# Kernel tuning notes

Hardware: AMD Instinct MI355X
Metric: run time of the kernel (lower is better)

The kernel has to match this reference:

```python
import jax, jax.numpy as jnp
import numpy as np

D_MODEL = 1024
N_HEADS = 16
WINDOW = 128
B, N, M = 2, 2048, 2048


def _linear_params(key, d_in, d_out):
    kw, kb = jax.random.split(key)
    lim = 1.0 / np.sqrt(d_in)
    w = jax.random.uniform(kw, (d_out, d_in), jnp.float32, -lim, lim)
    b = jax.random.uniform(kb, (d_out,), jnp.float32, -lim, lim)
    return w, b


def setup_inputs() -> dict:
    key = jax.random.key(0)
    ks = jax.random.split(key, 7)
    queries = jax.random.normal(ks[0], (B, N, D_MODEL), jnp.float32)
    keys = jax.random.normal(ks[1], (B, M, D_MODEL), jnp.float32)
    values = jax.random.normal(ks[2], (B, M, D_MODEL), jnp.float32)
    wq, bq = _linear_params(ks[3], D_MODEL, D_MODEL)
    wk, bk = _linear_params(ks[4], D_MODEL, D_MODEL)
    wv, bv = _linear_params(ks[5], D_MODEL, D_MODEL)
    wo, bo = _linear_params(ks[6], D_MODEL, D_MODEL)
    return {"queries": queries, "keys": keys, "values": values,
            "wq": wq, "bq": bq, "wk": wk, "bk": bk,
            "wv": wv, "bv": bv, "wo": wo, "bo": bo}


def reference(queries, keys, values, wq, bq, wk, bk, wv, bv, wo, bo):
    b, n, d = queries.shape
    m = keys.shape[1]
    h = N_HEADS
    hd = d // h
    scale = hd ** -0.5
    # torch Linear: y = x @ W.T + b
    q = (queries @ wq.T + bq).reshape(b, n, h, hd).transpose(0, 2, 1, 3)  # [B,H,N,hd]
    k = (keys @ wk.T + bk).reshape(b, m, h, hd).transpose(0, 2, 1, 3)     # [B,H,M,hd]
    v = (values @ wv.T + bv).reshape(b, m, h, hd).transpose(0, 2, 1, 3)   # [B,H,M,hd]
    logits = jnp.einsum('bhnd,bhmd->bhnm', q, k) * scale                   # [B,H,N,M]
    qi = jnp.arange(n)[:, None]
    ki = jnp.arange(m)[None, :]
    if m != n:
        ki = (ki.astype(jnp.float32) * n / max(m, 1)).astype(jnp.int32)
    local_mask = jnp.abs(qi - ki) > WINDOW // 2                            # [N,M]
    logits = jnp.where(local_mask[None, None], -jnp.inf, logits)
    attn = jax.nn.softmax(logits, axis=-1)
    out = jnp.einsum('bhnm,bhmd->bhnd', attn, v)                           # [B,H,N,hd]
    out = out.transpose(0, 2, 1, 3).reshape(b, n, d)
    return out @ wo.T + bo
```

## Files before the change

### kernel.cpp

```cpp
#include <hip/hip_runtime.h>
#include <math.h>


#define D_MODEL 1024
#define N_HEADS 16
#define HD      64
#define WHALF   64
#define BATCH   2
#define NQTOK   2048
#define MKTOK   2048

typedef float f32x4 __attribute__((ext_vector_type(4)));
typedef short s16x8 __attribute__((ext_vector_type(8)));

static __device__ __forceinline__ unsigned short f2bf(float x) {
  unsigned u = __float_as_uint(x);
  unsigned r = (u + 0x7fffu + ((u >> 16) & 1u)) >> 16;
  return (unsigned short)r;
}
static __device__ __forceinline__ float bf2f(unsigned short h) {
  return __uint_as_float(((unsigned)h) << 16);
}

__global__ __launch_bounds__(256)
void cvt_split(const float* __restrict__ in, unsigned short* __restrict__ hi,
               unsigned short* __restrict__ lo, int ngroups) {
  const int g = blockIdx.x * 256 + threadIdx.x;
  if (g >= ngroups) return;
  const float4 v0 = *(const float4*)(in + (size_t)g * 8);
  const float4 v1 = *(const float4*)(in + (size_t)g * 8 + 4);
  const float xs[8] = {v0.x, v0.y, v0.z, v0.w, v1.x, v1.y, v1.z, v1.w};
  unsigned short hs[8], ls[8];
#pragma unroll
  for (int i = 0; i < 8; ++i) {
    hs[i] = f2bf(xs[i]);
    ls[i] = f2bf(xs[i] - bf2f(hs[i]));
  }
  uint4 hv, lv;
  hv.x = (unsigned)hs[0] | ((unsigned)hs[1] << 16);
  hv.y = (unsigned)hs[2] | ((unsigned)hs[3] << 16);
  hv.z = (unsigned)hs[4] | ((unsigned)hs[5] << 16);
  hv.w = (unsigned)hs[6] | ((unsigned)hs[7] << 16);
  lv.x = (unsigned)ls[0] | ((unsigned)ls[1] << 16);
  lv.y = (unsigned)ls[2] | ((unsigned)ls[3] << 16);
  lv.z = (unsigned)ls[4] | ((unsigned)ls[5] << 16);
  lv.w = (unsigned)ls[6] | ((unsigned)ls[7] << 16);
  *(uint4*)(hi + (size_t)g * 8) = hv;
  *(uint4*)(lo + (size_t)g * 8) = lv;
}

#define TBM 128
#define TBN 64
#define TBK 32

__global__ __launch_bounds__(256)
void mfma_gemm(const unsigned short* __restrict__ Ah, const unsigned short* __restrict__ Al,
               const unsigned short* __restrict__ Bh, const unsigned short* __restrict__ Bl,
               const float* __restrict__ bias, float* __restrict__ C) {
  __shared__ unsigned short smem[12288];
  const int t  = threadIdx.x;
  const int wv = t >> 6;
  const int ln = t & 63;
  const int row0 = blockIdx.x * TBM;
  const int col0 = blockIdx.y * TBN;
  const int wr = wv >> 1, wc = wv & 1;

  f32x4 acc[4][2];
#pragma unroll
  for (int mi = 0; mi < 4; ++mi)
#pragma unroll
    for (int ni = 0; ni < 2; ++ni)
      acc[mi][ni] = (f32x4){0.f, 0.f, 0.f, 0.f};

  auto lds3 = (__attribute__((address_space(3))) unsigned short*)smem;

  for (int kt = 0; kt < D_MODEL / TBK; ++kt) {
    const int kb = kt * TBK;
    if (kt) __syncthreads();
#pragma unroll
    for (int cc = 0; cc < 6; ++cc) {
      const int c = wv * 6 + cc;
      const unsigned short* src;
      int dst, rowg;
      if (c < 8)       { src = Ah; dst = c * 512;              rowg = row0 + c * 16; }
      else if (c < 16) { src = Al; dst = 4096 + (c - 8) * 512; rowg = row0 + (c - 8) * 16; }
      else if (c < 20) { src = Bh; dst = 8192 + (c - 16) * 512; rowg = col0 + (c - 16) * 16; }
      else             { src = Bl; dst = 10240 + (c - 20) * 512; rowg = col0 + (c - 20) * 16; }
      const unsigned short* g =
          src + (size_t)(rowg + (ln >> 2)) * D_MODEL + kb + (ln & 3) * 8;
      __builtin_amdgcn_global_load_lds((const __attribute__((address_space(1))) void*)g,
                                       (__attribute__((address_space(3))) void*)(lds3 + dst),
                                       16, 0, 0);
    }
    __syncthreads();

    const int fr = ln & 15;
    const int ks = (ln >> 4) * 8;
    s16x8 a_h[4], a_l[4], b_h[2], b_l[2];
#pragma unroll
    for (int mi = 0; mi < 4; ++mi) {
      const int r = wr * 64 + mi * 16 + fr;
      a_h[mi] = *(const s16x8*)&smem[r * 32 + ks];
      a_l[mi] = *(const s16x8*)&smem[4096 + r * 32 + ks];
    }
#pragma unroll
    for (int ni = 0; ni < 2; ++ni) {
      const int r = wc * 32 + ni * 16 + fr;
      b_h[ni] = *(const s16x8*)&smem[8192 + r * 32 + ks];
      b_l[ni] = *(const s16x8*)&smem[10240 + r * 32 + ks];
    }
#pragma unroll
    for (int mi = 0; mi < 4; ++mi)
#pragma unroll
      for (int ni = 0; ni < 2; ++ni) {
        acc[mi][ni] = __builtin_amdgcn_mfma_f32_16x16x32_bf16(a_h[mi], b_h[ni], acc[mi][ni], 0, 0, 0);
        acc[mi][ni] = __builtin_amdgcn_mfma_f32_16x16x32_bf16(a_h[mi], b_l[ni], acc[mi][ni], 0, 0, 0);
        acc[mi][ni] = __builtin_amdgcn_mfma_f32_16x16x32_bf16(a_l[mi], b_h[ni], acc[mi][ni], 0, 0, 0);
      }
  }

  const int fr = ln & 15, fq = ln >> 4;
  float bval[2];
  bval[0] = bias[col0 + wc * 32 + fr];
  bval[1] = bias[col0 + wc * 32 + 16 + fr];
#pragma unroll
  for (int mi = 0; mi < 4; ++mi)
#pragma unroll
    for (int ni = 0; ni < 2; ++ni)
#pragma unroll
      for (int j = 0; j < 4; ++j) {
        const int r = row0 + wr * 64 + mi * 16 + fq * 4 + j;
        const int cg = col0 + wc * 32 + ni * 16 + fr;
        C[(size_t)r * D_MODEL + cg] = acc[mi][ni][j] + bval[ni];
      }
}

#define GBM 128
#define GBN 64
#define GBK 32
#define GSX 132
#define GSW 68

__global__ __launch_bounds__(256)
void proj_gemm(const float* __restrict__ X, const float* __restrict__ W,
               const float* __restrict__ bias, float* __restrict__ C) {
  __shared__ __align__(16) float Xs[GBK][GSX];
  __shared__ __align__(16) float Ws[GBK][GSW];
  const int t   = threadIdx.x;
  const int tx  = t & 15;
  const int ty  = t >> 4;
  const int row0 = blockIdx.x * GBM;
  const int col0 = blockIdx.y * GBN;
  float acc[8][4] = {};
  for (int kt = 0; kt < D_MODEL / GBK; ++kt) {
    const int kbase = kt * GBK;
    __syncthreads();
#pragma unroll
    for (int p = 0; p < 4; ++p) {
      const int idx = t + p * 256;
      const int r = idx >> 3, f = idx & 7;
      const float4 v = *(const float4*)(X + (size_t)(row0 + r) * D_MODEL + kbase + f * 4);
      Xs[f * 4 + 0][r] = v.x; Xs[f * 4 + 1][r] = v.y;
      Xs[f * 4 + 2][r] = v.z; Xs[f * 4 + 3][r] = v.w;
    }
#pragma unroll
    for (int p = 0; p < 2; ++p) {
      const int idx = t + p * 256;
      const int r = idx >> 3, f = idx & 7;
      const float4 v = *(const float4*)(W + (size_t)(col0 + r) * D_MODEL + kbase + f * 4);
      Ws[f * 4 + 0][r] = v.x; Ws[f * 4 + 1][r] = v.y;
      Ws[f * 4 + 2][r] = v.z; Ws[f * 4 + 3][r] = v.w;
    }
    __syncthreads();
#pragma unroll 4
    for (int kk = 0; kk < GBK; ++kk) {
      const float4 a0 = *(const float4*)&Xs[kk][ty * 8];
      const float4 a1 = *(const float4*)&Xs[kk][ty * 8 + 4];
      const float4 b  = *(const float4*)&Ws[kk][tx * 4];
      const float av[8] = {a0.x, a0.y, a0.z, a0.w, a1.x, a1.y, a1.z, a1.w};
      const float bv[4] = {b.x, b.y, b.z, b.w};
#pragma unroll
      for (int i = 0; i < 8; ++i)
#pragma unroll
        for (int j = 0; j < 4; ++j)
          acc[i][j] = fmaf(av[i], bv[j], acc[i][j]);
    }
  }
  const float4 b4 = *(const float4*)(bias + col0 + tx * 4);
#pragma unroll
  for (int i = 0; i < 8; ++i) {
    float4 o;
    o.x = acc[i][0] + b4.x; o.y = acc[i][1] + b4.y;
    o.z = acc[i][2] + b4.z; o.w = acc[i][3] + b4.w;
    *(float4*)(C + (size_t)(row0 + ty * 8 + i) * D_MODEL + col0 + tx * 4) = o;
  }
}

#define QB    32
#define CHUNK 80
#define KS    65
#define PS    161

__global__ __launch_bounds__(256)
void local_attn(const float* __restrict__ Q, const float* __restrict__ K,
                const float* __restrict__ V, float* __restrict__ AO,
                unsigned short* __restrict__ AOh, unsigned short* __restrict__ AOl,
                int split_out) {
  __shared__ float Qs[QB][KS];
  __shared__ float KVs[CHUNK][KS];
  __shared__ float P[QB][PS];
  __shared__ float inv_s[QB];

  const int t = threadIdx.x;
  const int nqb = NQTOK / QB;
  const int bid = blockIdx.x;
  const int qb  = bid % nqb;
  const int h   = (bid / nqb) % N_HEADS;
  const int b   = bid / (nqb * N_HEADS);
  const int q0  = qb * QB;
  const int j_lo = max(0, q0 - WHALF);
  const int j_hi = min(MKTOK - 1, q0 + QB - 1 + WHALF);
  const int KB   = j_hi - j_lo + 1;
  const float scale = 0.125f;

  const size_t base = (size_t)b * NQTOK * D_MODEL + h * HD;
  const float* Qb = Q + base;
  const float* Kb = K + base;
  const float* Vb = V + base;

  for (int idx = t; idx < QB * 16; idx += 256) {
    const int r = idx >> 4, f = idx & 15;
    const float4 v = *(const float4*)(Qb + (size_t)(q0 + r) * D_MODEL + f * 4);
    Qs[r][f * 4 + 0] = v.x * scale; Qs[r][f * 4 + 1] = v.y * scale;
    Qs[r][f * 4 + 2] = v.z * scale; Qs[r][f * 4 + 3] = v.w * scale;
  }

  const int txk = t & 15;
  const int tyq = t >> 4;
  for (int c = 0; c < 2; ++c) {
    const int jc0 = c * CHUNK;
    const int cnt = min(CHUNK, KB - jc0);
    __syncthreads();
    for (int idx = t; idx < cnt * 16; idx += 256) {
      const int r = idx >> 4, f = idx & 15;
      const float4 v = *(const float4*)(Kb + (size_t)(j_lo + jc0 + r) * D_MODEL + f * 4);
      KVs[r][f * 4 + 0] = v.x; KVs[r][f * 4 + 1] = v.y;
      KVs[r][f * 4 + 2] = v.z; KVs[r][f * 4 + 3] = v.w;
    }
    __syncthreads();
    float acc[2][5] = {};
#pragma unroll 4
    for (int d = 0; d < HD; ++d) {
      const float q0v = Qs[2 * tyq + 0][d];
      const float q1v = Qs[2 * tyq + 1][d];
#pragma unroll
      for (int kc = 0; kc < 5; ++kc) {
        const float kv = KVs[txk * 5 + kc][d];
        acc[0][kc] = fmaf(q0v, kv, acc[0][kc]);
        acc[1][kc] = fmaf(q1v, kv, acc[1][kc]);
      }
    }
#pragma unroll
    for (int qc = 0; qc < 2; ++qc)
#pragma unroll
      for (int kc = 0; kc < 5; ++kc)
        P[2 * tyq + qc][jc0 + txk * 5 + kc] = acc[qc][kc];
  }
  __syncthreads();

  {
    const int q = t >> 3, s8 = t & 7;
    const int qi = q0 + q;
    float mx = -1e30f;
    for (int jj = s8; jj < KB; jj += 8) {
      int diff = qi - (j_lo + jj); if (diff < 0) diff = -diff;
      if (diff <= WHALF) mx = fmaxf(mx, P[q][jj]);
    }
    mx = fmaxf(mx, __shfl_xor(mx, 1));
    mx = fmaxf(mx, __shfl_xor(mx, 2));
    mx = fmaxf(mx, __shfl_xor(mx, 4));
    float sum = 0.f;
    for (int jj = s8; jj < KB; jj += 8) {
      int diff = qi - (j_lo + jj); if (diff < 0) diff = -diff;
      float e = 0.f;
      if (diff <= WHALF) { e = expf(P[q][jj] - mx); sum += e; }
      P[q][jj] = e;
    }
    sum += __shfl_xor(sum, 1);
    sum += __shfl_xor(sum, 2);
    sum += __shfl_xor(sum, 4);
    if (s8 == 0) inv_s[q] = 1.f / sum;
  }

  const int d  = t & 63;
  const int qg = t >> 6;
  float oacc[8] = {};
  for (int c = 0; c < 2; ++c) {
    const int jc0 = c * CHUNK;
    const int cnt = min(CHUNK, KB - jc0);
    __syncthreads();
    for (int idx = t; idx < cnt * 16; idx += 256) {
      const int r = idx >> 4, f = idx & 15;
      const float4 v = *(const float4*)(Vb + (size_t)(j_lo + jc0 + r) * D_MODEL + f * 4);
      KVs[r][f * 4 + 0] = v.x; KVs[r][f * 4 + 1] = v.y;
      KVs[r][f * 4 + 2] = v.z; KVs[r][f * 4 + 3] = v.w;
    }
    __syncthreads();
    for (int jj = 0; jj < cnt; ++jj) {
      const float v = KVs[jj][d];
#pragma unroll
      for (int i = 0; i < 8; ++i)
        oacc[i] = fmaf(P[qg * 8 + i][jc0 + jj], v, oacc[i]);
    }
  }
#pragma unroll
  for (int i = 0; i < 8; ++i) {
    const int q = qg * 8 + i;
    const float o = oacc[i] * inv_s[q];
    const size_t off = base + (size_t)(q0 + q) * D_MODEL + d;
    if (split_out) {
      const unsigned short hh = f2bf(o);
      AOh[off] = hh;
      AOl[off] = f2bf(o - bf2f(hh));
    } else {
      AO[off] = o;
    }
  }
}

extern "C" void kernel_launch(void* const* d_in, const int* in_sizes, int n_in,
                              void* d_out, int out_size, void* d_ws, size_t ws_size,
                              hipStream_t stream) {
  const float* queries = (const float*)d_in[0];
  const float* keys    = (const float*)d_in[1];
  const float* values  = (const float*)d_in[2];
  const float* wq = (const float*)d_in[3];
  const float* bq = (const float*)d_in[4];
  const float* wk = (const float*)d_in[5];
  const float* bk = (const float*)d_in[6];
  const float* wv = (const float*)d_in[7];
  const float* bv = (const float*)d_in[8];
  const float* wo = (const float*)d_in[9];
  const float* bo = (const float*)d_in[10];
  float* out = (float*)d_out;

  const size_t mat  = (size_t)BATCH * NQTOK * D_MODEL;
  const size_t wmat = (size_t)D_MODEL * D_MODEL;
  const size_t need = 6 * mat * 2 + 8 * wmat * 2 + 3 * mat * 4;

  const dim3 attn_grid(BATCH * N_HEADS * (NQTOK / QB));

  if (ws_size >= need) {
    unsigned short* qh  = (unsigned short*)d_ws;
    unsigned short* ql  = qh + mat;
    unsigned short* kh  = ql + mat;
    unsigned short* kl  = kh + mat;
    unsigned short* vh  = kl + mat;
    unsigned short* vl  = vh + mat;
    unsigned short* wqh = vl + mat;
    unsigned short* wql = wqh + wmat;
    unsigned short* wkh = wql + wmat;
    unsigned short* wkl = wkh + wmat;
    unsigned short* wvh = wkl + wmat;
    unsigned short* wvl = wvh + wmat;
    unsigned short* woh = wvl + wmat;
    unsigned short* wol = woh + wmat;
    float* Qf = (float*)(wol + wmat);
    float* Kf = Qf + mat;
    float* Vf = Kf + mat;
    unsigned short* aoh = qh;
    unsigned short* aol = ql;

    cvt_split<<<dim3((unsigned)(mat / 2048)), 256, 0, stream>>>(queries, qh, ql, (int)(mat / 8));
    cvt_split<<<dim3((unsigned)(mat / 2048)), 256, 0, stream>>>(keys,    kh, kl, (int)(mat / 8));
    cvt_split<<<dim3((unsigned)(mat / 2048)), 256, 0, stream>>>(values,  vh, vl, (int)(mat / 8));
    cvt_split<<<dim3((unsigned)(wmat / 2048)), 256, 0, stream>>>(wq, wqh, wql, (int)(wmat / 8));
    cvt_split<<<dim3((unsigned)(wmat / 2048)), 256, 0, stream>>>(wk, wkh, wkl, (int)(wmat / 8));
    cvt_split<<<dim3((unsigned)(wmat / 2048)), 256, 0, stream>>>(wv, wvh, wvl, (int)(wmat / 8));
    cvt_split<<<dim3((unsigned)(wmat / 2048)), 256, 0, stream>>>(wo, woh, wol, (int)(wmat / 8));

    const dim3 gm(BATCH * NQTOK / TBM, D_MODEL / TBN);
    mfma_gemm<<<gm, 256, 0, stream>>>(qh, ql, wqh, wql, bq, Qf);
    mfma_gemm<<<gm, 256, 0, stream>>>(kh, kl, wkh, wkl, bk, Kf);
    mfma_gemm<<<gm, 256, 0, stream>>>(vh, vl, wvh, wvl, bv, Vf);

    local_attn<<<attn_grid, 256, 0, stream>>>(Qf, Kf, Vf, nullptr, aoh, aol, 1);

    mfma_gemm<<<gm, 256, 0, stream>>>(aoh, aol, woh, wol, bo, out);
  } else {
    float* Qws = (float*)d_ws;
    float* Kws = Qws + mat;
    float* Vws = Kws + mat;
    float* AOws = Qws;

    const dim3 gg(BATCH * NQTOK / GBM, D_MODEL / GBN);
    proj_gemm<<<gg, 256, 0, stream>>>(queries, wq, bq, Qws);
    proj_gemm<<<gg, 256, 0, stream>>>(keys,    wk, bk, Kws);
    proj_gemm<<<gg, 256, 0, stream>>>(values,  wv, bv, Vws);
    local_attn<<<attn_grid, 256, 0, stream>>>(Qws, Kws, Vws, AOws, nullptr, nullptr, 0);
    proj_gemm<<<gg, 256, 0, stream>>>(AOws, wo, bo, out);
  }
}
```

Baseline: 362.2 us.

## Use MFMA split-bf16 local attention with transposed V and fused conversions

Replaces the fp32 FMA-based local attention with an MFMA kernel that computes QK^T and PV using hi/lo bf16 split products, one wavefront per 32-query tile. The projection GEMMs now emit split bf16 directly, with V written transposed so PV fragments load contiguously, removing fp32 Q/K/V intermediates. The seven conversion launches are merged into one. This trades extra MFMA work (three products per tile) and the strided transposed V store for lower attention compute cost and less memory traffic.

```diff
diff --git a/kernel.cpp b/kernel.cpp
--- a/kernel.cpp
+++ b/kernel.cpp
@@ -12,41 +12,55 @@
 
 typedef float f32x4 __attribute__((ext_vector_type(4)));
 typedef short s16x8 __attribute__((ext_vector_type(8)));
-
-static __device__ __forceinline__ unsigned short f2bf(float x) {
+typedef unsigned short u16;
+
+static __device__ __forceinline__ u16 f2bf(float x) {
   unsigned u = __float_as_uint(x);
   unsigned r = (u + 0x7fffu + ((u >> 16) & 1u)) >> 16;
-  return (unsigned short)r;
-}
-static __device__ __forceinline__ float bf2f(unsigned short h) {
+  return (u16)r;
+}
+static __device__ __forceinline__ float bf2f(u16 h) {
   return __uint_as_float(((unsigned)h) << 16);
 }
 
+#define MAT  4194304u
+#define WMAT 1048576u
+
 __global__ __launch_bounds__(256)
-void cvt_split(const float* __restrict__ in, unsigned short* __restrict__ hi,
-               unsigned short* __restrict__ lo, int ngroups) {
-  const int g = blockIdx.x * 256 + threadIdx.x;
-  if (g >= ngroups) return;
-  const float4 v0 = *(const float4*)(in + (size_t)g * 8);
-  const float4 v1 = *(const float4*)(in + (size_t)g * 8 + 4);
+void cvt_all(const float* __restrict__ q, const float* __restrict__ k,
+             const float* __restrict__ v, const float* __restrict__ wq,
+             const float* __restrict__ wk, const float* __restrict__ wv,
+             const float* __restrict__ wo, u16* __restrict__ W) {
+  const unsigned g = blockIdx.x * 256 + threadIdx.x;
+  const float* src;
+  size_t dbase; unsigned off;
+  if (g < 524288u)        { src = q;  dbase = 0;                  off = g; }
+  else if (g < 1048576u)  { src = k;  dbase = 2u * MAT;           off = g - 524288u; }
+  else if (g < 1572864u)  { src = v;  dbase = 4u * MAT;           off = g - 1048576u; }
+  else if (g < 1703936u)  { src = wq; dbase = 6u * (size_t)MAT;               off = g - 1572864u; }
+  else if (g < 1835008u)  { src = wk; dbase = 6u * (size_t)MAT + 2u * WMAT;   off = g - 1703936u; }
+  else if (g < 1966080u)  { src = wv; dbase = 6u * (size_t)MAT + 4u * WMAT;   off = g - 1835008u; }
+  else                    { src = wo; dbase = 6u * (size_t)MAT + 6u * WMAT;   off = g - 1966080u; }
+  const size_t stride = (dbase < 6u * (size_t)MAT) ? MAT : WMAT;
+  u16* dh = W + dbase;
+  u16* dl = dh + stride;
+  const size_t e = (size_t)off * 8;
+  const float4 v0 = *(const float4*)(src + e);
+  const float4 v1 = *(const float4*)(src + e + 4);
   const float xs[8] = {v0.x, v0.y, v0.z, v0.w, v1.x, v1.y, v1.z, v1.w};
-  unsigned short hs[8], ls[8];
+  u16 hs[8], ls[8];
 #pragma unroll
   for (int i = 0; i < 8; ++i) {
     hs[i] = f2bf(xs[i]);
     ls[i] = f2bf(xs[i] - bf2f(hs[i]));
   }
   uint4 hv, lv;
-  hv.x = (unsigned)hs[0] | ((unsigned)hs[1] << 16);
-  hv.y = (unsigned)hs[2] | ((unsigned)hs[3] << 16);
-  hv.z = (unsigned)hs[4] | ((unsigned)hs[5] << 16);
-  hv.w = (unsigned)hs[6] | ((unsigned)hs[7] << 16);
-  lv.x = (unsigned)ls[0] | ((unsigned)ls[1] << 16);
-  lv.y = (unsigned)ls[2] | ((unsigned)ls[3] << 16);
-  lv.z = (unsigned)ls[4] | ((unsigned)ls[5] << 16);
-  lv.w = (unsigned)ls[6] | ((unsigned)ls[7] << 16);
-  *(uint4*)(hi + (size_t)g * 8) = hv;
-  *(uint4*)(lo + (size_t)g * 8) = lv;
+  hv.x = hs[0] | ((unsigned)hs[1] << 16); hv.y = hs[2] | ((unsigned)hs[3] << 16);
+  hv.z = hs[4] | ((unsigned)hs[5] << 16); hv.w = hs[6] | ((unsigned)hs[7] << 16);
+  lv.x = ls[0] | ((unsigned)ls[1] << 16); lv.y = ls[2] | ((unsigned)ls[3] << 16);
+  lv.z = ls[4] | ((unsigned)ls[5] << 16); lv.w = ls[6] | ((unsigned)ls[7] << 16);
+  *(uint4*)(dh + e) = hv;
+  *(uint4*)(dl + e) = lv;
 }
 
 #define TBM 128
@@ -54,10 +68,11 @@
 #define TBK 32
 
 __global__ __launch_bounds__(256)
-void mfma_gemm(const unsigned short* __restrict__ Ah, const unsigned short* __restrict__ Al,
-               const unsigned short* __restrict__ Bh, const unsigned short* __restrict__ Bl,
-               const float* __restrict__ bias, float* __restrict__ C) {
-  __shared__ unsigned short smem[12288];
+void mfma_gemm(const u16* __restrict__ Ah, const u16* __restrict__ Al,
+               const u16* __restrict__ Bh, const u16* __restrict__ Bl,
+               const float* __restrict__ bias, float* __restrict__ Cf,
+               u16* __restrict__ Ch, u16* __restrict__ Cl, int mode) {
+  __shared__ u16 smem[12288];
   const int t  = threadIdx.x;
   const int wv = t >> 6;
   const int ln = t & 63;
@@ -72,7 +87,7 @@
     for (int ni = 0; ni < 2; ++ni)
       acc[mi][ni] = (f32x4){0.f, 0.f, 0.f, 0.f};
 
-  auto lds3 = (__attribute__((address_space(3))) unsigned short*)smem;
+  auto lds3 = (__attribute__((address_space(3))) u16*)smem;
 
   for (int kt = 0; kt < D_MODEL / TBK; ++kt) {
     const int kb = kt * TBK;
@@ -80,14 +95,13 @@
 #pragma unroll
     for (int cc = 0; cc < 6; ++cc) {
       const int c = wv * 6 + cc;
-      const unsigned short* src;
+      const u16* src;
       int dst, rowg;
-      if (c < 8)       { src = Ah; dst = c * 512;              rowg = row0 + c * 16; }
-      else if (c < 16) { src = Al; dst = 4096 + (c - 8) * 512; rowg = row0 + (c - 8) * 16; }
+      if (c < 8)       { src = Ah; dst = c * 512;               rowg = row0 + c * 16; }
+      else if (c < 16) { src = Al; dst = 4096 + (c - 8) * 512;  rowg = row0 + (c - 8) * 16; }
       else if (c < 20) { src = Bh; dst = 8192 + (c - 16) * 512; rowg = col0 + (c - 16) * 16; }
       else             { src = Bl; dst = 10240 + (c - 20) * 512; rowg = col0 + (c - 20) * 16; }
-      const unsigned short* g =
-          src + (size_t)(rowg + (ln >> 2)) * D_MODEL + kb + (ln & 3) * 8;
+      const u16* g = src + (size_t)(rowg + (ln >> 2)) * D_MODEL + kb + (ln & 3) * 8;
       __builtin_amdgcn_global_load_lds((const __attribute__((address_space(1))) void*)g,
                                        (__attribute__((address_space(3))) void*)(lds3 + dst),
                                        16, 0, 0);
@@ -129,9 +143,164 @@
     for (int ni = 0; ni < 2; ++ni)
 #pragma unroll
       for (int j = 0; j < 4; ++j) {
-        const int r = row0 + wr * 64 + mi * 16 + fq * 4 + j;
+        const int r  = row0 + wr * 64 + mi * 16 + fq * 4 + j;
         const int cg = col0 + wc * 32 + ni * 16 + fr;
-        C[(size_t)r * D_MODEL + cg] = acc[mi][ni][j] + bval[ni];
+        const float o = acc[mi][ni][j] + bval[ni];
+        if (mode == 0) {
+          Cf[(size_t)r * D_MODEL + cg] = o;
+        } else {
+          size_t idx;
+          if (mode == 1) idx = (size_t)r * D_MODEL + cg;
+          else           idx = ((size_t)(r >> 11) * D_MODEL + cg) * (size_t)MKTOK + (r & 2047);
+          const u16 hb = f2bf(o);
+          Ch[idx] = hb;
+          Cl[idx] = f2bf(o - bf2f(hb));
+        }
+      }
+}
+
+__global__ __launch_bounds__(256)
+void mfma_attn(const u16* __restrict__ Qh, const u16* __restrict__ Ql,
+               const u16* __restrict__ Kh, const u16* __restrict__ Kl,
+               const u16* __restrict__ Vth, const u16* __restrict__ Vtl,
+               u16* __restrict__ AOh, u16* __restrict__ AOl) {
+  __shared__ __align__(16) u16 Pbuf[4][2][32 * 40];
+  const int t = threadIdx.x, w = t >> 6, ln = t & 63;
+  const int fr = ln & 15, fq = ln >> 4;
+  int bb = blockIdx.x;
+  bb = (bb & 7) * 64 + (bb >> 3);
+  const int g  = bb * 4 + w;
+  const int qt = g & 63, h = (g >> 6) & 15, b = g >> 10;
+  const int q0 = qt * 32;
+  const int jlo = (q0 >= WHALF) ? q0 - WHALF : 0;
+  const size_t tb = (size_t)b * NQTOK * D_MODEL;
+  const int hc = h * HD;
+
+  s16x8 qf[2][2][2];
+#pragma unroll
+  for (int mt = 0; mt < 2; ++mt)
+#pragma unroll
+    for (int kt = 0; kt < 2; ++kt) {
+      const size_t o = tb + (size_t)(q0 + mt * 16 + fr) * D_MODEL + hc + kt * 32 + fq * 8;
+      qf[mt][kt][0] = *(const s16x8*)(Qh + o);
+      qf[mt][kt][1] = *(const s16x8*)(Ql + o);
+    }
+
+  f32x4 L[2][10];
+#pragma unroll
+  for (int mt = 0; mt < 2; ++mt)
+#pragma unroll
+    for (int nt = 0; nt < 10; ++nt) L[mt][nt] = (f32x4){0.f, 0.f, 0.f, 0.f};
+#pragma unroll
+  for (int nt = 0; nt < 10; ++nt) {
+    int jr = jlo + nt * 16 + fr;
+    if (jr > MKTOK - 1) jr = MKTOK - 1;
+#pragma unroll
+    for (int kt = 0; kt < 2; ++kt) {
+      const size_t o = tb + (size_t)jr * D_MODEL + hc + kt * 32 + fq * 8;
+      const s16x8 kfh = *(const s16x8*)(Kh + o);
+      const s16x8 kfl = *(const s16x8*)(Kl + o);
+#pragma unroll
+      for (int mt = 0; mt < 2; ++mt) {
+        L[mt][nt] = __builtin_amdgcn_mfma_f32_16x16x32_bf16(qf[mt][kt][0], kfh, L[mt][nt], 0, 0, 0);
+        L[mt][nt] = __builtin_amdgcn_mfma_f32_16x16x32_bf16(qf[mt][kt][0], kfl, L[mt][nt], 0, 0, 0);
+        L[mt][nt] = __builtin_amdgcn_mfma_f32_16x16x32_bf16(qf[mt][kt][1], kfh, L[mt][nt], 0, 0, 0);
+      }
+    }
+  }
+
+  float inv[2][4];
+#pragma unroll
+  for (int mt = 0; mt < 2; ++mt)
+#pragma unroll
+    for (int rg = 0; rg < 4; ++rg) {
+      const int q = q0 + mt * 16 + fq * 4 + rg;
+      float mx = -3.0e38f;
+#pragma unroll
+      for (int nt = 0; nt < 10; ++nt) {
+        const int j = jlo + nt * 16 + fr;
+        const int d = q - j;
+        const bool ok = (d <= WHALF) && (d >= -WHALF) && (j < MKTOK);
+        const float lv = ok ? L[mt][nt][rg] * 0.125f : -3.0e38f;
+        L[mt][nt][rg] = lv;
+        mx = fmaxf(mx, lv);
+      }
+      mx = fmaxf(mx, __shfl_xor(mx, 1));
+      mx = fmaxf(mx, __shfl_xor(mx, 2));
+      mx = fmaxf(mx, __shfl_xor(mx, 4));
+      mx = fmaxf(mx, __shfl_xor(mx, 8));
+      float sm = 0.f;
+#pragma unroll
+      for (int nt = 0; nt < 10; ++nt) {
+        const float lv = L[mt][nt][rg];
+        const float e = (lv > -1.0e38f) ? __expf(lv - mx) : 0.f;
+        L[mt][nt][rg] = e;
+        sm += e;
+      }
+      sm += __shfl_xor(sm, 1);
+      sm += __shfl_xor(sm, 2);
+      sm += __shfl_xor(sm, 4);
+      sm += __shfl_xor(sm, 8);
+      inv[mt][rg] = 1.f / sm;
+    }
+
+  f32x4 oacc[2][4];
+#pragma unroll
+  for (int mt = 0; mt < 2; ++mt)
+#pragma unroll
+    for (int nt = 0; nt < 4; ++nt) oacc[mt][nt] = (f32x4){0.f, 0.f, 0.f, 0.f};
+
+  u16* ph = &Pbuf[w][0][0];
+  u16* pl = &Pbuf[w][1][0];
+#pragma unroll
+  for (int c = 0; c < 5; ++c) {
+    __syncthreads();
+#pragma unroll
+    for (int mt = 0; mt < 2; ++mt)
+#pragma unroll
+      for (int half = 0; half < 2; ++half) {
+        const int nt = 2 * c + half;
+#pragma unroll
+        for (int rg = 0; rg < 4; ++rg) {
+          const float v = L[mt][nt][rg] * inv[mt][rg];
+          const u16 hb = f2bf(v);
+          const int idx = (mt * 16 + fq * 4 + rg) * 40 + half * 16 + fr;
+          ph[idx] = hb;
+          pl[idx] = f2bf(v - bf2f(hb));
+        }
+      }
+    __syncthreads();
+#pragma unroll
+    for (int mt = 0; mt < 2; ++mt) {
+      const s16x8 pfh = *(const s16x8*)&ph[(mt * 16 + fr) * 40 + fq * 8];
+      const s16x8 pfl = *(const s16x8*)&pl[(mt * 16 + fr) * 40 + fq * 8];
+      int tk = jlo + c * 32 + fq * 8;
+      if (tk > MKTOK - 8) tk = MKTOK - 8;
+#pragma unroll
+      for (int nt = 0; nt < 4; ++nt) {
+        const size_t o = ((size_t)b * D_MODEL + hc + nt * 16 + fr) * (size_t)MKTOK + tk;
+        const s16x8 vfh = *(const s16x8*)(Vth + o);
+        const s16x8 vfl = *(const s16x8*)(Vtl + o);
+        oacc[mt][nt] = __builtin_amdgcn_mfma_f32_16x16x32_bf16(pfh, vfh, oacc[mt][nt], 0, 0, 0);
+        oacc[mt][nt] = __builtin_amdgcn_mfma_f32_16x16x32_bf16(pfh, vfl, oacc[mt][nt], 0, 0, 0);
+        oacc[mt][nt] = __builtin_amdgcn_mfma_f32_16x16x32_bf16(pfl, vfh, oacc[mt][nt], 0, 0, 0);
+      }
+    }
+  }
+
+#pragma unroll
+  for (int mt = 0; mt < 2; ++mt)
+#pragma unroll
+    for (int nt = 0; nt < 4; ++nt)
+#pragma unroll
+      for (int j = 0; j < 4; ++j) {
+        const int q = q0 + mt * 16 + fq * 4 + j;
+        const int d = hc + nt * 16 + fr;
+        const float o = oacc[mt][nt][j];
+        const size_t idx = tb + (size_t)q * D_MODEL + d;
+        const u16 hb = f2bf(o);
+        AOh[idx] = hb;
+        AOl[idx] = f2bf(o - bf2f(hb));
       }
 }
 
@@ -203,14 +372,11 @@
 
 __global__ __launch_bounds__(256)
 void local_attn(const float* __restrict__ Q, const float* __restrict__ K,
-                const float* __restrict__ V, float* __restrict__ AO,
-                unsigned short* __restrict__ AOh, unsigned short* __restrict__ AOl,
-                int split_out) {
+                const float* __restrict__ V, float* __restrict__ AO) {
   __shared__ float Qs[QB][KS];
   __shared__ float KVs[CHUNK][KS];
   __shared__ float P[QB][PS];
   __shared__ float inv_s[QB];
-
   const int t = threadIdx.x;
   const int nqb = NQTOK / QB;
   const int bid = blockIdx.x;
@@ -222,19 +388,16 @@
   const int j_hi = min(MKTOK - 1, q0 + QB - 1 + WHALF);
   const int KB   = j_hi - j_lo + 1;
   const float scale = 0.125f;
-
   const size_t base = (size_t)b * NQTOK * D_MODEL + h * HD;
   const float* Qb = Q + base;
   const float* Kb = K + base;
   const float* Vb = V + base;
-
   for (int idx = t; idx < QB * 16; idx += 256) {
     const int r = idx >> 4, f = idx & 15;
     const float4 v = *(const float4*)(Qb + (size_t)(q0 + r) * D_MODEL + f * 4);
     Qs[r][f * 4 + 0] = v.x * scale; Qs[r][f * 4 + 1] = v.y * scale;
     Qs[r][f * 4 + 2] = v.z * scale; Qs[r][f * 4 + 3] = v.w * scale;
   }
-
   const int txk = t & 15;
   const int tyq = t >> 4;
   for (int c = 0; c < 2; ++c) {
@@ -267,7 +430,6 @@
         P[2 * tyq + qc][jc0 + txk * 5 + kc] = acc[qc][kc];
   }
   __syncthreads();
-
   {
     const int q = t >> 3, s8 = t & 7;
     const int qi = q0 + q;
@@ -291,7 +453,6 @@
     sum += __shfl_xor(sum, 4);
     if (s8 == 0) inv_s[q] = 1.f / sum;
   }
-
   const int d  = t & 63;
   const int qg = t >> 6;
   float oacc[8] = {};
@@ -316,15 +477,7 @@
 #pragma unroll
   for (int i = 0; i < 8; ++i) {
     const int q = qg * 8 + i;
-    const float o = oacc[i] * inv_s[q];
-    const size_t off = base + (size_t)(q0 + q) * D_MODEL + d;
-    if (split_out) {
-      const unsigned short hh = f2bf(o);
-      AOh[off] = hh;
-      AOl[off] = f2bf(o - bf2f(hh));
-    } else {
-      AO[off] = o;
-    }
+    AO[base + (size_t)(q0 + q) * D_MODEL + d] = oacc[i] * inv_s[q];
   }
 }
 
@@ -344,60 +497,49 @@
   const float* bo = (const float*)d_in[10];
   float* out = (float*)d_out;
 
-  const size_t mat  = (size_t)BATCH * NQTOK * D_MODEL;
-  const size_t wmat = (size_t)D_MODEL * D_MODEL;
-  const size_t need = 6 * mat * 2 + 8 * wmat * 2 + 3 * mat * 4;
-
-  const dim3 attn_grid(BATCH * N_HEADS * (NQTOK / QB));
+  const size_t mat  = MAT;
+  const size_t wmat = WMAT;
+  const size_t need = 117440512;
 
   if (ws_size >= need) {
-    unsigned short* qh  = (unsigned short*)d_ws;
-    unsigned short* ql  = qh + mat;
-    unsigned short* kh  = ql + mat;
-    unsigned short* kl  = kh + mat;
-    unsigned short* vh  = kl + mat;
-    unsigned short* vl  = vh + mat;
-    unsigned short* wqh = vl + mat;
-    unsigned short* wql = wqh + wmat;
-    unsigned short* wkh = wql + wmat;
-    unsigned short* wkl = wkh + wmat;
-    unsigned short* wvh = wkl + wmat;
-    unsigned short* wvl = wvh + wmat;
-    unsigned short* woh = wvl + wmat;
-    unsigned short* wol = woh + wmat;
-    float* Qf = (float*)(wol + wmat);
-    float* Kf = Qf + mat;
-    float* Vf = Kf + mat;
-    unsigned short* aoh = qh;
-    unsigned short* aol = ql;
-
-    cvt_split<<<dim3((unsigned)(mat / 2048)), 256, 0, stream>>>(queries, qh, ql, (int)(mat / 8));
-    cvt_split<<<dim3((unsigned)(mat / 2048)), 256, 0, stream>>>(keys,    kh, kl, (int)(mat / 8));
-    cvt_split<<<dim3((unsigned)(mat / 2048)), 256, 0, stream>>>(values,  vh, vl, (int)(mat / 8));
-    cvt_split<<<dim3((unsigned)(wmat / 2048)), 256, 0, stream>>>(wq, wqh, wql, (int)(wmat / 8));
-    cvt_split<<<dim3((unsigned)(wmat / 2048)), 256, 0, stream>>>(wk, wkh, wkl, (int)(wmat / 8));
-    cvt_split<<<dim3((unsigned)(wmat / 2048)), 256, 0, stream>>>(wv, wvh, wvl, (int)(wmat / 8));
-    cvt_split<<<dim3((unsigned)(wmat / 2048)), 256, 0, stream>>>(wo, woh, wol, (int)(wmat / 8));
+    u16* W = (u16*)d_ws;
+    u16* xqh = W;
+    u16* xql = xqh + mat;
+    u16* xkh = W + 2 * mat;
+    u16* xkl = xkh + mat;
+    u16* xvh = W + 4 * mat;
+    u16* xvl = xvh + mat;
+    u16* wgt = W + 6 * mat;
+    u16* wqh = wgt;             u16* wql = wgt + wmat;
+    u16* wkh = wgt + 2 * wmat;  u16* wkl = wgt + 3 * wmat;
+    u16* wvh = wgt + 4 * wmat;  u16* wvl = wgt + 5 * wmat;
+    u16* woh = wgt + 6 * wmat;  u16* wol = wgt + 7 * wmat;
+    u16* outs = wgt + 8 * wmat;
+    u16* qh  = outs;            u16* ql  = outs + mat;
+    u16* kh  = outs + 2 * mat;  u16* kl  = outs + 3 * mat;
+    u16* vth = outs + 4 * mat;  u16* vtl = outs + 5 * mat;
+    u16* aoh = xqh;             u16* aol = xql;
+
+    cvt_all<<<dim3(8192), 256, 0, stream>>>(queries, keys, values, wq, wk, wv, wo, W);
 
     const dim3 gm(BATCH * NQTOK / TBM, D_MODEL / TBN);
-    mfma_gemm<<<gm, 256, 0, stream>>>(qh, ql, wqh, wql, bq, Qf);
-    mfma_gemm<<<gm, 256, 0, stream>>>(kh, kl, wkh, wkl, bk, Kf);
-    mfma_gemm<<<gm, 256, 0, stream>>>(vh, vl, wvh, wvl, bv, Vf);
-
-    local_attn<<<attn_grid, 256, 0, stream>>>(Qf, Kf, Vf, nullptr, aoh, aol, 1);
-
-    mfma_gemm<<<gm, 256, 0, stream>>>(aoh, aol, woh, wol, bo, out);
+    mfma_gemm<<<gm, 256, 0, stream>>>(xqh, xql, wqh, wql, bq, nullptr, qh, ql, 1);
+    mfma_gemm<<<gm, 256, 0, stream>>>(xkh, xkl, wkh, wkl, bk, nullptr, kh, kl, 1);
+    mfma_gemm<<<gm, 256, 0, stream>>>(xvh, xvl, wvh, wvl, bv, nullptr, vth, vtl, 2);
+
+    mfma_attn<<<dim3(512), 256, 0, stream>>>(qh, ql, kh, kl, vth, vtl, aoh, aol);
+
+    mfma_gemm<<<gm, 256, 0, stream>>>(aoh, aol, woh, wol, bo, out, nullptr, nullptr, 0);
   } else {
     float* Qws = (float*)d_ws;
     float* Kws = Qws + mat;
     float* Vws = Kws + mat;
     float* AOws = Qws;
-
     const dim3 gg(BATCH * NQTOK / GBM, D_MODEL / GBN);
     proj_gemm<<<gg, 256, 0, stream>>>(queries, wq, bq, Qws);
     proj_gemm<<<gg, 256, 0, stream>>>(keys,    wk, bk, Kws);
     proj_gemm<<<gg, 256, 0, stream>>>(values,  wv, bv, Vws);
-    local_attn<<<attn_grid, 256, 0, stream>>>(Qws, Kws, Vws, AOws, nullptr, nullptr, 0);
+    local_attn<<<dim3(BATCH * N_HEADS * (NQTOK / QB)), 256, 0, stream>>>(Qws, Kws, Vws, AOws);
     proj_gemm<<<gg, 256, 0, stream>>>(AOws, wo, bo, out);
   }
 }
```

Result: faster. 301.5 us (-16.7%).
